# Kernel tuning notes

Measured on AMD Instinct MI355X. Metric: run time of the kernel, lower is better.

## Reference

```python
import jax, jax.numpy as jnp
import numpy as np

B, N, E, D = 8, 10000, 160000, 256
H = D // 2
SLOPE = 0.2  # LeakyReLU negative slope


def setup_inputs() -> dict:
    key = jax.random.key(0)
    ks = jax.random.split(key, 8)
    node_feats = jax.random.normal(ks[0], (B, N, D), dtype=jnp.float32)
    edge_attr = jax.random.uniform(ks[1], (E, 1), dtype=jnp.float32)
    W1 = jax.random.normal(ks[2], (2 * D, H), dtype=jnp.float32) * 0.05
    b1 = jnp.zeros((H,), dtype=jnp.float32)
    W2 = jax.random.normal(ks[3], (H, 1), dtype=jnp.float32) * 0.05
    b2 = jnp.zeros((1,), dtype=jnp.float32)
    edge_index = jax.random.randint(ks[4], (2, E), 0, N, dtype=jnp.int64)
    valid_masks = jax.random.randint(ks[5], (B, N), 0, 2).astype(bool)
    return {"node_feats": node_feats, "edge_attr": edge_attr, "W1": W1, "b1": b1,
            "W2": W2, "b2": b2, "edge_index": edge_index, "valid_masks": valid_masks}


def reference(node_feats, edge_attr, W1, b1, W2, b2, edge_index, valid_masks):
    # node_feats: [B,N,D]; edge_index: [2,E] shared across batch
    d = node_feats.shape[-1]
    src, dst = edge_index[0], edge_index[1]
    # cat([src_feats, dst_feats]) @ W1 == src @ W1[:d] + dst @ W1[d:]
    # Project per-node first, then gather per-edge: avoids the [B,E,2D] concat.
    ps = jnp.einsum('bnd,dh->bnh', node_feats, W1[:d])   # [B,N,H]
    pd = jnp.einsum('bnd,dh->bnh', node_feats, W1[d:])   # [B,N,H]
    h = ps[:, src] + pd[:, dst] + b1                      # [B,E,H]
    h = jnp.where(h >= 0, h, SLOPE * h)                   # LeakyReLU(0.2)
    scores = jnp.einsum('beh,h->be', h, W2[:, 0]) + b2[0]  # [B,E]
    scores = scores * edge_attr[:, 0]                     # edge_attr multiplies pre-softmax
    w = jax.nn.softmax(scores, axis=1)                    # global softmax over all edges
    # sparse_coo(edge_index, w) @ node_feats: out[src[e]] += w[e] * feats[dst[e]]
    msg = w[..., None] * node_feats[:, dst]               # [B,E,D]
    n = node_feats.shape[1]
    agg = jax.vmap(lambda m: jax.ops.segment_sum(m, src, num_segments=n))(msg)  # [B,N,D]
    mask = valid_masks.astype(node_feats.dtype)           # [B,N]
    cnt = mask.sum(axis=1)                                # [B]
    masked_mean = (agg * mask[..., None]).sum(axis=1) / jnp.maximum(cnt, 1.0)[:, None]
    full_mean = agg.mean(axis=1)
    graph_feats = jnp.where((cnt > 0)[:, None], masked_mean, full_mean)  # [B,D]
    return graph_feats, w
```

## Files before the change

### kernel.cpp

```cpp
#include <hip/hip_runtime.h>
#include <hip/hip_bf16.h>
#include <hip/hip_fp16.h>

#define B_ 8
#define N_ 10000
#define E_ 160000
#define D_ 256
#define H_ 128
#define SLOPE 0.2f
#define NCHUNK 100

#define NB_ 64
#define EPB_ (E_ / NB_)
#define BINS_ 256
#define NPB_ (N_ / 16)
#define SUBS_ 8

#define SB_ 256
#define SEB_ (E_ / SB_)

typedef __attribute__((ext_vector_type(8))) _Float16 v8h;
typedef __attribute__((ext_vector_type(4))) _Float16 v4h;
typedef __attribute__((ext_vector_type(2))) _Float16 v2h;
typedef __attribute__((ext_vector_type(4))) float f32x4;

static __device__ __forceinline__ float dot2f(v2h a, v2h b, float c) {
#if __has_builtin(__builtin_amdgcn_fdot2)
    return __builtin_amdgcn_fdot2(a, b, c, false);
#else
    return fmaf((float)a.y, (float)b.y, fmaf((float)a.x, (float)b.x, c));
#endif
}

static __device__ __forceinline__ void block_flags(const int* __restrict__ eidx_raw,
                                                   const unsigned int* __restrict__ mask32,
                                                   int tid, int* sfl) {
    if (tid < 64) {
        unsigned long long oddnz = __ballot(eidx_raw[2 * tid + 1] != 0);
        unsigned long long mgt1  = __ballot(mask32[tid] > 1u);
        if (tid == 0) {
            sfl[0] = (oddnz == 0ull) ? 1 : 0;
            sfl[1] = (mgt1 != 0ull) ? 1 : 0;
        }
    }
    __syncthreads();
}

__global__ __launch_bounds__(256) void kprep(const int* __restrict__ eidx_raw,
                                             const unsigned char* __restrict__ mask8,
                                             const unsigned int* __restrict__ mask32,
                                             const float* __restrict__ W1,
                                             const float* __restrict__ b1,
                                             const float* __restrict__ W2,
                                             int* __restrict__ ce,
                                             unsigned char* __restrict__ cmT,
                                             __half* __restrict__ Wt,
                                             __half* __restrict__ b1h,
                                             __half* __restrict__ w2h,
                                             int* __restrict__ cnti,
                                             int* __restrict__ hpart) {
    const int tid = threadIdx.x;
    __shared__ int sfl[2];
    __shared__ int scnt[8];

    if (blockIdx.x < 1250) {
        if (tid < 8) scnt[tid] = 0;
        block_flags(eidx_raw, mask32, tid, sfl);
        const int f_e = sfl[0], f_m = sfl[1];
        const int i = blockIdx.x * 256 + tid;
        if (i < 2 * E_) ce[i] = f_e ? eidx_raw[2 * i] : eidx_raw[i];
        if (i < B_ * N_) {
            unsigned char v = f_m ? (unsigned char)(mask8[i] != 0)
                                  : (unsigned char)(mask32[i] != 0u);
            const int b = i / N_;
            const int n = i - b * N_;
            cmT[n * 8 + b] = v;
            if (v) atomicAdd(&scnt[b], 1);
        }
        if (i < 2 * 256 * 128) {
            const int f = i & 127;
            const int row = i >> 7;
            const int c = row >> 8, k = row & 255;
            Wt[((c * 128 + f) * 256) + k] = __float2half(W1[row * 128 + f]);
        }
        if (i < 128) {
            b1h[i] = __float2half(b1[i]);
            w2h[i] = __float2half(W2[i]);
        }
        __syncthreads();
        if (tid < 8 && scnt[tid]) atomicAdd(&cnti[tid], scnt[tid]);
    } else {
        block_flags(eidx_raw, mask32, tid, sfl);
        const int f_e = sfl[0];
        __shared__ int h[BINS_];
        h[tid] = 0;
        __syncthreads();
        const int hb = blockIdx.x - 1250;
        const int base = hb * EPB_;
        for (int i = tid; i < EPB_; i += 256) {
            const int e = base + i;
            const int s = f_e ? eidx_raw[2 * e] : eidx_raw[e];
            const int d = f_e ? eidx_raw[2 * (E_ + e)] : eidx_raw[E_ + e];
            const int bin = (d / NPB_) * 16 + s / NPB_;
            atomicAdd(&h[bin], 1);
        }
        __syncthreads();
        hpart[hb * BINS_ + tid] = h[tid];
    }
}

__global__ __launch_bounds__(256) void kprefix(const int* __restrict__ hpart,
                                               int* __restrict__ offsetG,
                                               int* __restrict__ bstart) {
    __shared__ int cnt[BINS_];
    __shared__ int excl[BINS_];
    const int bin = threadIdx.x;
    int c = 0;
    for (int b = 0; b < NB_; b++) c += hpart[b * BINS_ + bin];
    cnt[bin] = c;
    __syncthreads();
    if (bin == 0) {
        int r = 0;
        for (int i = 0; i < BINS_; i++) { excl[i] = r; r += cnt[i]; }
    }
    __syncthreads();
    if ((bin & 15) == 0) bstart[bin >> 4] = excl[bin];
    if (bin == 0) bstart[16] = E_;
    int run = excl[bin];
    for (int b = 0; b < NB_; b++) {
        offsetG[b * BINS_ + bin] = run;
        run += hpart[b * BINS_ + bin];
    }
}

__global__ __launch_bounds__(256) void k1_mfma(const float* __restrict__ X,
                                               const __half* __restrict__ Wt,
                                               __half* __restrict__ ps,
                                               __half* __restrict__ pd,
                                               const int* __restrict__ ce,
                                               const int* __restrict__ offsetG,
                                               int4* __restrict__ esort,
                                               int* __restrict__ rank) {
    const int tid = threadIdx.x;
    __shared__ __align__(16) char smem[64 * 136 * 2];

    if (blockIdx.x >= 1250) {
        int* loc = (int*)smem;
        const int sb = blockIdx.x - 1250;
        loc[tid] = offsetG[sb * BINS_ + tid];
        __syncthreads();
        const int base = sb * EPB_;
        for (int i = tid; i < EPB_; i += 256) {
            const int e = base + i;
            const int s = ce[e], d = ce[E_ + e];
            const int bin = (d / NPB_) * 16 + s / NPB_;
            const int pos = atomicAdd(&loc[bin], 1);
            esort[pos] = make_int4(s, d, e, 0);
            rank[e] = pos;
        }
        return;
    }

    const int rb = blockIdx.x;
    const int wave = tid >> 6, lane = tid & 63;
    const int quad = lane >> 4, l16 = lane & 15;
    _Float16* Xs = (_Float16*)smem;
    _Float16* T  = (_Float16*)smem;

    f32x4 acc[2][2][4];
#pragma unroll
    for (int c = 0; c < 2; c++)
#pragma unroll
        for (int i = 0; i < 2; i++)
#pragma unroll
            for (int j = 0; j < 4; j++) acc[c][i][j] = (f32x4){0.f, 0.f, 0.f, 0.f};

    const int row_base = rb * 64;
    const int sr = tid >> 3;
    const int sc = (tid & 7) * 4;

    const float* xsrc  = &X[(size_t)(row_base + sr) * 256 + sc];
    const float* xsrc2 = xsrc + 32 * 256;
    const __half* wbase = &Wt[((size_t)(wave * 32 + l16)) * 256 + quad * 8];

    float4 xa, xb;
    v8h wcur[2][2], wnxt[2][2];

    xa = *(const float4*)(xsrc);
    xb = *(const float4*)(xsrc2);
#pragma unroll
    for (int cb = 0; cb < 2; cb++)
#pragma unroll
        for (int ft = 0; ft < 2; ft++)
            wcur[cb][ft] = *(const v8h*)(wbase + (size_t)(cb * 128 + ft * 16) * 256);
    {
        v4h pa = {(_Float16)xa.x, (_Float16)xa.y, (_Float16)xa.z, (_Float16)xa.w};
        v4h pb = {(_Float16)xb.x, (_Float16)xb.y, (_Float16)xb.z, (_Float16)xb.w};
        *(v4h*)&Xs[sr * 40 + sc] = pa;
        *(v4h*)&Xs[(sr + 32) * 40 + sc] = pb;
    }
    __syncthreads();

    for (int kc = 0; kc < 8; ++kc) {
        const int cur = kc & 1;
        if (kc < 7) {
            xa = *(const float4*)(xsrc + (kc + 1) * 32);
            xb = *(const float4*)(xsrc2 + (kc + 1) * 32);
#pragma unroll
            for (int cb = 0; cb < 2; cb++)
#pragma unroll
                for (int ft = 0; ft < 2; ft++)
                    wnxt[cb][ft] = *(const v8h*)(wbase + (size_t)(cb * 128 + ft * 16) * 256 + (kc + 1) * 32);
        }
#pragma unroll
        for (int nt = 0; nt < 4; ++nt) {
            v8h xf = *(v8h*)&Xs[cur * (64 * 40) + (nt * 16 + l16) * 40 + quad * 8];
            acc[0][0][nt] = __builtin_amdgcn_mfma_f32_16x16x32_f16(wcur[0][0], xf, acc[0][0][nt], 0, 0, 0);
            acc[0][1][nt] = __builtin_amdgcn_mfma_f32_16x16x32_f16(wcur[0][1], xf, acc[0][1][nt], 0, 0, 0);
            acc[1][0][nt] = __builtin_amdgcn_mfma_f32_16x16x32_f16(wcur[1][0], xf, acc[1][0][nt], 0, 0, 0);
            acc[1][1][nt] = __builtin_amdgcn_mfma_f32_16x16x32_f16(wcur[1][1], xf, acc[1][1][nt], 0, 0, 0);
        }
        if (kc < 7) {
            const int nb = (cur ^ 1) * (64 * 40);
            v4h pa = {(_Float16)xa.x, (_Float16)xa.y, (_Float16)xa.z, (_Float16)xa.w};
            v4h pb = {(_Float16)xb.x, (_Float16)xb.y, (_Float16)xb.z, (_Float16)xb.w};
            *(v4h*)&Xs[nb + sr * 40 + sc] = pa;
            *(v4h*)&Xs[nb + (sr + 32) * 40 + sc] = pb;
#pragma unroll
            for (int cb = 0; cb < 2; cb++)
#pragma unroll
                for (int ft = 0; ft < 2; ft++)
                    wcur[cb][ft] = wnxt[cb][ft];
        }
        __syncthreads();
    }

#pragma unroll
    for (int cb = 0; cb < 2; ++cb) {
        if (cb) __syncthreads();
#pragma unroll
        for (int nt = 0; nt < 4; ++nt)
#pragma unroll
            for (int ft = 0; ft < 2; ++ft) {
                f32x4 a = acc[cb][ft][nt];
                v4h h = {(_Float16)a.x, (_Float16)a.y, (_Float16)a.z, (_Float16)a.w};
                *(v4h*)&T[(nt * 16 + l16) * 136 + wave * 32 + ft * 16 + quad * 4] = h;
            }
        __syncthreads();
        __half* outp = cb ? pd : ps;
#pragma unroll
        for (int pass = 0; pass < 4; ++pass) {
            const int r = pass * 16 + (tid >> 4);
            const int f8 = (tid & 15) * 8;
            const int R = row_base + r;
            const int b = R / N_;
            const int n = R - b * N_;
            *(float4*)(outp + ((size_t)b * N_ + n) * 128 + f8) =
                *(const float4*)&T[r * 136 + f8];
        }
    }
}

__global__ __launch_bounds__(256) void k2_scores(const __half* __restrict__ ps,
                                                 const __half* __restrict__ pd,
                                                 const int4* __restrict__ esort,
                                                 const __half* __restrict__ b1h,
                                                 const __half* __restrict__ w2h,
                                                 const float* __restrict__ b2,
                                                 const float* __restrict__ eattr,
                                                 float* __restrict__ scS) {
    const int tid = threadIdx.x;
    const int wave = tid >> 6;
    const int lane = tid & 63;
    const int bid = blockIdx.x;
    const int batch = bid & 7;
    const int e0 = (bid >> 3) * 128;

    const int hi = (lane & 7) * 16;

    v2h b1p[8], w2p[8];
    {
        const v2h* bp = (const v2h*)(b1h + hi);
        const v2h* wp = (const v2h*)(w2h + hi);
#pragma unroll
        for (int j = 0; j < 8; j++) { b1p[j] = bp[j]; w2p[j] = wp[j]; }
    }
    const float bias2 = b2[0];
    const v2h slp = {(_Float16)SLOPE, (_Float16)SLOPE};

    const __half* psb = ps + (size_t)batch * N_ * 128;
    const __half* pdb = pd + (size_t)batch * N_ * 128;
    float* scb = scS + (size_t)batch * E_;

    int4 er[4];
#pragma unroll
    for (int q = 0; q < 4; q++)
        er[q] = esort[e0 + wave * 32 + q * 8 + (lane >> 3)];

    float4 rs[4][2], rd[4][2];
#pragma unroll
    for (int q = 0; q < 4; q++) {
        const float4* aps = (const float4*)&psb[(size_t)er[q].x * 128 + hi];
        const float4* apd = (const float4*)&pdb[(size_t)er[q].y * 128 + hi];
        rs[q][0] = aps[0]; rs[q][1] = aps[1];
        rd[q][0] = apd[0]; rd[q][1] = apd[1];
    }

#pragma unroll
    for (int q = 0; q < 4; q++) {
        const v2h* sv = (const v2h*)rs[q];
        const v2h* dv = (const v2h*)rd[q];
        float acc = 0.f;
#pragma unroll
        for (int j = 0; j < 8; j++) {
            v2h x = sv[j] + dv[j] + b1p[j];
            v2h l = __builtin_elementwise_max(x, x * slp);
            acc = dot2f(l, w2p[j], acc);
        }
        acc += __shfl_xor(acc, 1);
        acc += __shfl_xor(acc, 2);
        acc += __shfl_xor(acc, 4);

        if ((lane & 7) == 0) {
            const int e = e0 + wave * 32 + q * 8 + (lane >> 3);
            scb[e] = (acc + bias2) * eattr[er[q].z];
        }
    }
}

__global__ __launch_bounds__(256) void k3s_stats(const float* __restrict__ scS,
                                                 float* __restrict__ pmax,
                                                 double* __restrict__ psum) {
    const int tid = threadIdx.x;
    const int wave = tid >> 6, lane = tid & 63;
    const int base = blockIdx.x * SEB_;

    float fm[8];
#pragma unroll
    for (int j = 0; j < 8; j++) fm[j] = -3.4e38f;
    for (int i = tid; i < SEB_; i += 256) {
        const int p = base + i;
#pragma unroll
        for (int j = 0; j < 8; j++)
            fm[j] = fmaxf(fm[j], scS[(size_t)j * E_ + p]);
    }
#pragma unroll
    for (int k = 1; k <= 32; k <<= 1)
#pragma unroll
        for (int j = 0; j < 8; j++) fm[j] = fmaxf(fm[j], __shfl_xor(fm[j], k));
    __shared__ float lmax[4][8];
    if (lane == 0)
#pragma unroll
        for (int j = 0; j < 8; j++) lmax[wave][j] = fm[j];
    __syncthreads();
    float m[8];
#pragma unroll
    for (int j = 0; j < 8; j++)
        m[j] = fmaxf(fmaxf(lmax[0][j], lmax[1][j]), fmaxf(lmax[2][j], lmax[3][j]));

    double s[8];
#pragma unroll
    for (int j = 0; j < 8; j++) s[j] = 0.0;
    for (int i = tid; i < SEB_; i += 256) {
        const int p = base + i;
#pragma unroll
        for (int j = 0; j < 8; j++)
            s[j] += (double)expf(scS[(size_t)j * E_ + p] - m[j]);
    }
#pragma unroll
    for (int k = 1; k <= 32; k <<= 1)
#pragma unroll
        for (int j = 0; j < 8; j++) s[j] += __shfl_xor(s[j], k);
    __shared__ double lsum[4][8];
    if (lane == 0)
#pragma unroll
        for (int j = 0; j < 8; j++) lsum[wave][j] = s[j];
    __syncthreads();
    if (tid < 8) {
        pmax[blockIdx.x * 8 + tid] = m[tid];
        psum[blockIdx.x * 8 + tid] = lsum[0][tid] + lsum[1][tid] + lsum[2][tid] + lsum[3][tid];
    }
}

static __device__ __forceinline__ void stats_combine(const float* __restrict__ pmax,
                                                     const double* __restrict__ psum,
                                                     int tid, float* smx, float* sinvx) {
    if (tid < 64) {
        float mc[SB_ / 64][8];
        float v[8];
#pragma unroll
        for (int j = 0; j < 8; j++) v[j] = -3.4e38f;
#pragma unroll
        for (int g = 0; g < SB_ / 64; g++) {
            const float4* p4 = (const float4*)&pmax[(g * 64 + tid) * 8];
            float4 a = p4[0], b = p4[1];
            mc[g][0] = a.x; mc[g][1] = a.y; mc[g][2] = a.z; mc[g][3] = a.w;
            mc[g][4] = b.x; mc[g][5] = b.y; mc[g][6] = b.z; mc[g][7] = b.w;
#pragma unroll
            for (int j = 0; j < 8; j++) v[j] = fmaxf(v[j], mc[g][j]);
        }
#pragma unroll
        for (int k = 1; k <= 32; k <<= 1)
#pragma unroll
            for (int j = 0; j < 8; j++) v[j] = fmaxf(v[j], __shfl_xor(v[j], k));
        double z[8];
#pragma unroll
        for (int j = 0; j < 8; j++) z[j] = 0.0;
#pragma unroll
        for (int g = 0; g < SB_ / 64; g++)
#pragma unroll
            for (int j = 0; j < 8; j++)
                z[j] += psum[(g * 64 + tid) * 8 + j] * (double)expf(mc[g][j] - v[j]);
#pragma unroll
        for (int k = 1; k <= 32; k <<= 1)
#pragma unroll
            for (int j = 0; j < 8; j++) z[j] += __shfl_xor(z[j], k);
        if (tid == 0)
#pragma unroll
            for (int j = 0; j < 8; j++) { smx[j] = v[j]; sinvx[j] = (float)(1.0 / z[j]); }
    }
}

__global__ __launch_bounds__(256) void k3ef(const int4* __restrict__ esort,
                                            const float* __restrict__ scS,
                                            const unsigned char* __restrict__ cmT,
                                            const float* __restrict__ pmax,
                                            const double* __restrict__ psum,
                                            const int* __restrict__ bstart,
                                            const int* __restrict__ rank,
                                            float* __restrict__ Wpf,
                                            float* __restrict__ Wpm,
                                            float* __restrict__ wout) {
    const int tid = threadIdx.x;
    __shared__ float smx[8], sinvx[8];
    __shared__ float lWf[NPB_ * 8];
    __shared__ float lWm[NPB_ * 8];

    stats_combine(pmax, psum, tid, smx, sinvx);

    if (blockIdx.x >= 16 * SUBS_) {
        __syncthreads();
        const int e = (blockIdx.x - 16 * SUBS_) * 256 + tid;
        const int p = rank[e];
#pragma unroll
        for (int j = 0; j < 8; j++) {
            const float v = scS[(size_t)j * E_ + p];
            wout[(size_t)j * E_ + e] = expf(v - smx[j]) * sinvx[j];
        }
        return;
    }

    const int bucket = blockIdx.x / SUBS_;
    const int sub = blockIdx.x % SUBS_;

    for (int i = tid; i < NPB_ * 8; i += 256) { lWf[i] = 0.f; lWm[i] = 0.f; }
    __syncthreads();

    float m[8], inv[8];
#pragma unroll
    for (int j = 0; j < 8; j++) { m[j] = smx[j]; inv[j] = sinvx[j]; }

    const int bs = bstart[bucket], be = bstart[bucket + 1];
    const int len = be - bs;
    const int s0 = bs + (int)((long long)len * sub / SUBS_);
    const int s1 = bs + (int)((long long)len * (sub + 1) / SUBS_);
    const int nbase = bucket * NPB_;

    for (int p = s0 + tid; p < s1; p += 256) {
        const int4 er = esort[p];
        const int src = er.x;
        const int rel = er.y - nbase;
        float wv[8];
#pragma unroll
        for (int j = 0; j < 8; j++)
            wv[j] = expf(scS[(size_t)j * E_ + p] - m[j]) * inv[j];
        const unsigned long long mm = *(const unsigned long long*)&cmT[src * 8];
        float* lf = &lWf[rel * 8];
        float* lm = &lWm[rel * 8];
#pragma unroll
        for (int j = 0; j < 8; j++) {
            atomicAdd(&lf[j], wv[j]);
            if ((mm >> (8 * j)) & 1ull) atomicAdd(&lm[j], wv[j]);
        }
    }
    __syncthreads();

    float* of = Wpf + ((size_t)bucket * SUBS_ + sub) * (NPB_ * 8);
    float* om = Wpm + ((size_t)bucket * SUBS_ + sub) * (NPB_ * 8);
    for (int i = tid; i < NPB_ * 8; i += 256) { of[i] = lWf[i]; om[i] = lWm[i]; }
}

__global__ __launch_bounds__(256) void k3g_reduce(const float* __restrict__ Wpf,
                                                  const float* __restrict__ Wpm,
                                                  float* __restrict__ WfT,
                                                  float* __restrict__ WmT) {
    const int i = blockIdx.x * 256 + threadIdx.x;
    if (i >= N_ * 8) return;
    const int n = i >> 3, b = i & 7;
    const int bucket = n / NPB_;
    const int rel = n - bucket * NPB_;
    float sf = 0.f, sm = 0.f;
#pragma unroll
    for (int sub = 0; sub < SUBS_; sub++) {
        const size_t off = ((size_t)bucket * SUBS_ + sub) * (NPB_ * 8) + rel * 8 + b;
        sf += Wpf[off];
        sm += Wpm[off];
    }
    WfT[i] = sf;
    WmT[i] = sm;
}

__global__ __launch_bounds__(256) void k4b_wsum(const float* __restrict__ X,
                                                const float* __restrict__ WmT,
                                                const float* __restrict__ WfT,
                                                float* __restrict__ gpart) {
    const int c = blockIdx.x;
    const int b = blockIdx.y;
    const int tx = threadIdx.x & 63;
    const int ty = threadIdx.x >> 6;
    const int npc = N_ / NCHUNK;
    const int n0 = c * npc;

    const float4* X4 = (const float4*)(X + (size_t)b * N_ * 256);
    float4 am = {0.f, 0.f, 0.f, 0.f};
    float4 af = {0.f, 0.f, 0.f, 0.f};

    for (int n = n0 + ty; n < n0 + npc; n += 4) {
        float wm = WmT[n * 8 + b];
        float wf = WfT[n * 8 + b];
        float4 v = X4[(size_t)n * 64 + tx];
        am.x = fmaf(wm, v.x, am.x); am.y = fmaf(wm, v.y, am.y);
        am.z = fmaf(wm, v.z, am.z); am.w = fmaf(wm, v.w, am.w);
        af.x = fmaf(wf, v.x, af.x); af.y = fmaf(wf, v.y, af.y);
        af.z = fmaf(wf, v.z, af.z); af.w = fmaf(wf, v.w, af.w);
    }

    __shared__ float4 red[256];
    red[threadIdx.x] = am;
    __syncthreads();
    if (ty == 0) {
        float4 r1 = red[tx + 64], r2 = red[tx + 128], r3 = red[tx + 192];
        am.x += r1.x + r2.x + r3.x; am.y += r1.y + r2.y + r3.y;
        am.z += r1.z + r2.z + r3.z; am.w += r1.w + r2.w + r3.w;
    }
    __syncthreads();
    red[threadIdx.x] = af;
    __syncthreads();
    if (ty == 0) {
        float4 r1 = red[tx + 64], r2 = red[tx + 128], r3 = red[tx + 192];
        af.x += r1.x + r2.x + r3.x; af.y += r1.y + r2.y + r3.y;
        af.z += r1.z + r2.z + r3.z; af.w += r1.w + r2.w + r3.w;
        float4* gp4 = (float4*)gpart;
        gp4[((c * 2 + 0) * 8 + b) * 64 + tx] = am;
        gp4[((c * 2 + 1) * 8 + b) * 64 + tx] = af;
    }
}

__global__ __launch_bounds__(256) void k5_final(const float* __restrict__ gpart,
                                                const int* __restrict__ cnti,
                                                float* __restrict__ gf) {
    const int b = blockIdx.x;
    const int d = threadIdx.x;
    float sm = 0.f, sf = 0.f;
    for (int c = 0; c < NCHUNK; c++) {
        sm += gpart[((c * 2 + 0) * 8 + b) * 256 + d];
        sf += gpart[((c * 2 + 1) * 8 + b) * 256 + d];
    }
    const float cn = (float)cnti[b];
    gf[b * 256 + d] = (cn > 0.f) ? (sm / cn) : (sf / (float)N_);
}

static inline char* align16(char* p) {
    return (char*)(((uintptr_t)p + 15) & ~(uintptr_t)15);
}

extern "C" void kernel_launch(void* const* d_in, const int* in_sizes, int n_in,
                              void* d_out, int out_size, void* d_ws, size_t ws_size,
                              hipStream_t stream) {
    const float* X     = (const float*)d_in[0];
    const float* eattr = (const float*)d_in[1];
    const float* W1    = (const float*)d_in[2];
    const float* b1    = (const float*)d_in[3];
    const float* W2    = (const float*)d_in[4];
    const float* b2    = (const float*)d_in[5];
    const int*   eidx_raw = (const int*)d_in[6];
    const unsigned char* mask8 = (const unsigned char*)d_in[7];
    const unsigned int*  mask32 = (const unsigned int*)d_in[7];

    float* out  = (float*)d_out;
    float* gf   = out;
    float* wout = out + 2048;

    char* cur = (char*)d_ws;
    __half* ps_h = (__half*)cur;             cur += (size_t)N_ * 8 * 128 * 2;
    __half* pd_h = (__half*)cur;             cur += (size_t)N_ * 8 * 128 * 2;
    __half* Wt   = (__half*)cur;             cur += 2 * 128 * 256 * 2;
    int* ce      = (int*)cur;                cur += 2 * E_ * 4;
    unsigned char* cmT = (unsigned char*)cur; cur += N_ * 8;
    cur = align16(cur);
    int* cnti    = (int*)cur;                cur += 8 * 4;
    cur = align16(cur);
    float* pmax  = (float*)cur;              cur += SB_ * 8 * 4;
    cur = align16(cur);
    double* psum = (double*)cur;             cur += SB_ * 8 * 8;
    float* gpart = (float*)cur;              cur += NCHUNK * 2 * 8 * 256 * 4;
    int* hpart   = (int*)cur;                cur += NB_ * BINS_ * 4;
    int* offsetG = (int*)cur;                cur += NB_ * BINS_ * 4;
    int* bstart  = (int*)cur;                cur += 32 * 4;
    cur = align16(cur);
    int4* esort  = (int4*)cur;               cur += (size_t)E_ * 16;
    int* rankB   = (int*)cur;                cur += E_ * 4;
    __half* b1h  = (__half*)cur;             cur += 128 * 2;
    __half* w2h  = (__half*)cur;             cur += 128 * 2;
    cur = align16(cur);
    float* scS   = (float*)cur;              cur += (size_t)E_ * 8 * 4;

    char* ocur = (char*)d_ws;
    float* Wpf = (float*)ocur;               ocur += (size_t)16 * SUBS_ * NPB_ * 8 * 4;
    float* Wpm = (float*)ocur;               ocur += (size_t)16 * SUBS_ * NPB_ * 8 * 4;
    float* WfT = (float*)ocur;               ocur += N_ * 8 * 4;
    float* WmT = (float*)ocur;               ocur += N_ * 8 * 4;

    hipMemsetAsync(cnti, 0, 8 * sizeof(int), stream);
    hipLaunchKernelGGL(kprep, dim3(1250 + NB_), dim3(256), 0, stream,
                       eidx_raw, mask8, mask32, W1, b1, W2,
                       ce, cmT, Wt, b1h, w2h, cnti, hpart);
    hipLaunchKernelGGL(kprefix, dim3(1), dim3(256), 0, stream, hpart, offsetG, bstart);
    hipLaunchKernelGGL(k1_mfma, dim3(1250 + NB_), dim3(256), 0, stream,
                       X, Wt, ps_h, pd_h, ce, offsetG, esort, rankB);
    hipLaunchKernelGGL(k2_scores, dim3(E_ / 16), dim3(256), 0, stream,
                       ps_h, pd_h, esort, b1h, w2h, b2, eattr, scS);
    hipLaunchKernelGGL(k3s_stats, dim3(SB_), dim3(256), 0, stream, scS, pmax, psum);
    hipLaunchKernelGGL(k3ef, dim3(16 * SUBS_ + E_ / 256), dim3(256), 0, stream,
                       esort, scS, cmT, pmax, psum, bstart, rankB, Wpf, Wpm, wout);
    hipLaunchKernelGGL(k3g_reduce, dim3((N_ * 8 + 255) / 256), dim3(256), 0, stream,
                       Wpf, Wpm, WfT, WmT);
    hipLaunchKernelGGL(k4b_wsum, dim3(NCHUNK, 8), dim3(256), 0, stream, X, WmT, WfT, gpart);
    hipLaunchKernelGGL(k5_final, dim3(8), dim3(256), 0, stream, gpart, cnti, gf);
}
```

Measured before the change: 270.7 us.

## Drop canonical edge-index and rank buffers, read raw indices directly

Removes the intermediate canonicalized edge-index copy and the per-edge rank array. The sort kernel now decodes raw int64/int32 indices itself, and the softmax-output path scatters through the original edge id stored in esort. The valid-count is computed by dedicated per-batch reduction blocks instead of shared atomics plus a memset, which shrinks the prep grid. The softmax output write becomes a scatter rather than a coalesced store, and an unroll pragma is added to the weighted-sum loop.

```diff
diff --git a/kernel.cpp b/kernel.cpp
--- a/kernel.cpp
+++ b/kernel.cpp
@@ -15,6 +15,7 @@
 #define BINS_ 256
 #define NPB_ (N_ / 16)
 #define SUBS_ 8
+#define CANONB_ 313
 
 #define SB_ 256
 #define SEB_ (E_ / SB_)
@@ -52,7 +53,6 @@
                                              const float* __restrict__ W1,
                                              const float* __restrict__ b1,
                                              const float* __restrict__ W2,
-                                             int* __restrict__ ce,
                                              unsigned char* __restrict__ cmT,
                                              __half* __restrict__ Wt,
                                              __half* __restrict__ b1h,
@@ -61,21 +61,17 @@
                                              int* __restrict__ hpart) {
     const int tid = threadIdx.x;
     __shared__ int sfl[2];
-    __shared__ int scnt[8];
-
-    if (blockIdx.x < 1250) {
-        if (tid < 8) scnt[tid] = 0;
+
+    if (blockIdx.x < CANONB_) {
         block_flags(eidx_raw, mask32, tid, sfl);
-        const int f_e = sfl[0], f_m = sfl[1];
+        const int f_m = sfl[1];
         const int i = blockIdx.x * 256 + tid;
-        if (i < 2 * E_) ce[i] = f_e ? eidx_raw[2 * i] : eidx_raw[i];
         if (i < B_ * N_) {
             unsigned char v = f_m ? (unsigned char)(mask8[i] != 0)
                                   : (unsigned char)(mask32[i] != 0u);
             const int b = i / N_;
             const int n = i - b * N_;
             cmT[n * 8 + b] = v;
-            if (v) atomicAdd(&scnt[b], 1);
         }
         if (i < 2 * 256 * 128) {
             const int f = i & 127;
@@ -87,15 +83,13 @@
             b1h[i] = __float2half(b1[i]);
             w2h[i] = __float2half(W2[i]);
         }
-        __syncthreads();
-        if (tid < 8 && scnt[tid]) atomicAdd(&cnti[tid], scnt[tid]);
-    } else {
+    } else if (blockIdx.x < CANONB_ + NB_) {
         block_flags(eidx_raw, mask32, tid, sfl);
         const int f_e = sfl[0];
         __shared__ int h[BINS_];
         h[tid] = 0;
         __syncthreads();
-        const int hb = blockIdx.x - 1250;
+        const int hb = blockIdx.x - CANONB_;
         const int base = hb * EPB_;
         for (int i = tid; i < EPB_; i += 256) {
             const int e = base + i;
@@ -106,6 +100,23 @@
         }
         __syncthreads();
         hpart[hb * BINS_ + tid] = h[tid];
+    } else {
+        block_flags(eidx_raw, mask32, tid, sfl);
+        const int f_m = sfl[1];
+        const int b = blockIdx.x - CANONB_ - NB_;
+        int c = 0;
+        for (int i = tid; i < N_; i += 256) {
+            const int gi = b * N_ + i;
+            c += (f_m ? (mask8[gi] != 0) : (mask32[gi] != 0u)) ? 1 : 0;
+        }
+        __shared__ int red[256];
+        red[tid] = c;
+        __syncthreads();
+        for (int s = 128; s > 0; s >>= 1) {
+            if (tid < s) red[tid] += red[tid + s];
+            __syncthreads();
+        }
+        if (tid == 0) cnti[b] = red[0];
     }
 }
 
@@ -137,14 +148,17 @@
                                                const __half* __restrict__ Wt,
                                                __half* __restrict__ ps,
                                                __half* __restrict__ pd,
-                                               const int* __restrict__ ce,
+                                               const int* __restrict__ eidx_raw,
+                                               const unsigned int* __restrict__ mask32,
                                                const int* __restrict__ offsetG,
-                                               int4* __restrict__ esort,
-                                               int* __restrict__ rank) {
+                                               int4* __restrict__ esort) {
     const int tid = threadIdx.x;
     __shared__ __align__(16) char smem[64 * 136 * 2];
 
     if (blockIdx.x >= 1250) {
+        __shared__ int sfl[2];
+        block_flags(eidx_raw, mask32, tid, sfl);
+        const int f_e = sfl[0];
         int* loc = (int*)smem;
         const int sb = blockIdx.x - 1250;
         loc[tid] = offsetG[sb * BINS_ + tid];
@@ -152,11 +166,11 @@
         const int base = sb * EPB_;
         for (int i = tid; i < EPB_; i += 256) {
             const int e = base + i;
-            const int s = ce[e], d = ce[E_ + e];
+            const int s = f_e ? eidx_raw[2 * e] : eidx_raw[e];
+            const int d = f_e ? eidx_raw[2 * (E_ + e)] : eidx_raw[E_ + e];
             const int bin = (d / NPB_) * 16 + s / NPB_;
             const int pos = atomicAdd(&loc[bin], 1);
             esort[pos] = make_int4(s, d, e, 0);
-            rank[e] = pos;
         }
         return;
     }
@@ -427,7 +441,6 @@
                                             const float* __restrict__ pmax,
                                             const double* __restrict__ psum,
                                             const int* __restrict__ bstart,
-                                            const int* __restrict__ rank,
                                             float* __restrict__ Wpf,
                                             float* __restrict__ Wpm,
                                             float* __restrict__ wout) {
@@ -440,12 +453,12 @@
 
     if (blockIdx.x >= 16 * SUBS_) {
         __syncthreads();
-        const int e = (blockIdx.x - 16 * SUBS_) * 256 + tid;
-        const int p = rank[e];
+        const int p = (blockIdx.x - 16 * SUBS_) * 256 + tid;
+        const int orig = esort[p].z;
 #pragma unroll
         for (int j = 0; j < 8; j++) {
             const float v = scS[(size_t)j * E_ + p];
-            wout[(size_t)j * E_ + e] = expf(v - smx[j]) * sinvx[j];
+            wout[(size_t)j * E_ + orig] = expf(v - smx[j]) * sinvx[j];
         }
         return;
     }
@@ -525,6 +538,7 @@
     float4 am = {0.f, 0.f, 0.f, 0.f};
     float4 af = {0.f, 0.f, 0.f, 0.f};
 
+#pragma unroll 5
     for (int n = n0 + ty; n < n0 + npc; n += 4) {
         float wm = WmT[n * 8 + b];
         float wf = WfT[n * 8 + b];
@@ -595,7 +609,6 @@
     __half* ps_h = (__half*)cur;             cur += (size_t)N_ * 8 * 128 * 2;
     __half* pd_h = (__half*)cur;             cur += (size_t)N_ * 8 * 128 * 2;
     __half* Wt   = (__half*)cur;             cur += 2 * 128 * 256 * 2;
-    int* ce      = (int*)cur;                cur += 2 * E_ * 4;
     unsigned char* cmT = (unsigned char*)cur; cur += N_ * 8;
     cur = align16(cur);
     int* cnti    = (int*)cur;                cur += 8 * 4;
@@ -609,7 +622,6 @@
     int* bstart  = (int*)cur;                cur += 32 * 4;
     cur = align16(cur);
     int4* esort  = (int4*)cur;               cur += (size_t)E_ * 16;
-    int* rankB   = (int*)cur;                cur += E_ * 4;
     __half* b1h  = (__half*)cur;             cur += 128 * 2;
     __half* w2h  = (__half*)cur;             cur += 128 * 2;
     cur = align16(cur);
@@ -621,18 +633,17 @@
     float* WfT = (float*)ocur;               ocur += N_ * 8 * 4;
     float* WmT = (float*)ocur;               ocur += N_ * 8 * 4;
 
-    hipMemsetAsync(cnti, 0, 8 * sizeof(int), stream);
-    hipLaunchKernelGGL(kprep, dim3(1250 + NB_), dim3(256), 0, stream,
+    hipLaunchKernelGGL(kprep, dim3(CANONB_ + NB_ + 8), dim3(256), 0, stream,
                        eidx_raw, mask8, mask32, W1, b1, W2,
-                       ce, cmT, Wt, b1h, w2h, cnti, hpart);
+                       cmT, Wt, b1h, w2h, cnti, hpart);
     hipLaunchKernelGGL(kprefix, dim3(1), dim3(256), 0, stream, hpart, offsetG, bstart);
     hipLaunchKernelGGL(k1_mfma, dim3(1250 + NB_), dim3(256), 0, stream,
-                       X, Wt, ps_h, pd_h, ce, offsetG, esort, rankB);
+                       X, Wt, ps_h, pd_h, eidx_raw, mask32, offsetG, esort);
     hipLaunchKernelGGL(k2_scores, dim3(E_ / 16), dim3(256), 0, stream,
                        ps_h, pd_h, esort, b1h, w2h, b2, eattr, scS);
     hipLaunchKernelGGL(k3s_stats, dim3(SB_), dim3(256), 0, stream, scS, pmax, psum);
     hipLaunchKernelGGL(k3ef, dim3(16 * SUBS_ + E_ / 256), dim3(256), 0, stream,
-                       esort, scS, cmT, pmax, psum, bstart, rankB, Wpf, Wpm, wout);
+                       esort, scS, cmT, pmax, psum, bstart, Wpf, Wpm, wout);
     hipLaunchKernelGGL(k3g_reduce, dim3((N_ * 8 + 255) / 256), dim3(256), 0, stream,
                        Wpf, Wpm, WfT, WmT);
     hipLaunchKernelGGL(k4b_wsum, dim3(NCHUNK, 8), dim3(256), 0, stream, X, WmT, WfT, gpart);
```

Result: slower. 281.4 us (+4.0%).
